# Kernel tuning notes

Measured on AMD Instinct MI355X. Metric: run time of the kernel, lower is better.

The kernel has to match this reference:

```python
import jax, jax.numpy as jnp
import numpy as np

BS = 16384      # batch of tree nodes
N_CH = 8        # children per node (= max_output_degree)
H = 256         # h_size
RANK = 16       # tensor-train rank
N_AGGR = 4      # parallel aggregators
T = 64          # t_size (type embedding dim)
SCALE = 0.05    # param init scale (keeps the length-8 matmul chain stable)


def setup_inputs() -> dict:
    key = jax.random.key(0)
    ks = jax.random.split(key, 8)
    R = (RANK + 1) * RANK
    return {
        "neighbour_h": jax.random.normal(ks[0], (BS, N_CH, H), jnp.float32),
        "type_embs": jax.random.normal(ks[1], (BS, T), jnp.float32),
        "U": jax.random.normal(ks[2], (N_CH, N_AGGR, H, R), jnp.float32) * SCALE,
        "b": jax.random.normal(ks[3], (N_CH, N_AGGR, 1, R), jnp.float32) * SCALE,
        "U_type": jax.random.normal(ks[4], (N_AGGR, T, RANK), jnp.float32) * SCALE,
        "b_type": jax.random.normal(ks[5], (N_AGGR, 1, RANK), jnp.float32) * SCALE,
        "U_output": jax.random.normal(ks[6], (N_AGGR, RANK, H), jnp.float32) * SCALE,
        "b_output": jax.random.normal(ks[7], (N_AGGR, 1, H), jnp.float32) * SCALE,
    }


def reference(neighbour_h, type_embs, U, b, U_type, b_type, U_output, b_output):
    bs, n_ch, h = neighbour_h.shape
    n_aggr, _, rank = U_type.shape

    # per-child projection to TT cores: [bs, n_ch, n_aggr, (rank+1)*rank]
    ris = jnp.einsum('bch,cahr->bcar', neighbour_h, U[:n_ch]) + b[:n_ch, :, 0, :]
    ris = ris.reshape(bs, n_ch, n_aggr, rank + 1, rank)

    # initial rank vector from type embeddings: [bs, n_aggr, rank]
    rank_ris0 = jnp.einsum('bt,atr->bar', type_embs, U_type) + b_type[:, 0, :]

    # sequential TT chain over children (loop-carried dependency) via scan
    xs = jnp.moveaxis(ris, 1, 0)  # [n_ch, bs, n_aggr, rank+1, rank]

    def step(carry, aux):
        U_rank = aux[:, :, :-1, :]   # [bs, n_aggr, rank, rank]
        b_rank = aux[:, :, -2, :]    # row -2 (matches torch's aux[:,:,-2:-1,:])
        return jnp.einsum('bar,barq->baq', carry, U_rank) + b_rank, None

    rank_ris, _ = jax.lax.scan(step, rank_ris0, xs)

    # output projection: [bs, n_aggr, h]
    out = jnp.einsum('bar,arh->bah', rank_ris, U_output) + b_output[:, 0, :]
    return out.reshape(bs, n_aggr * h)
```

## Files before the change

kernel.cpp:

```cpp
#include <hip/hip_runtime.h>


#define N_CH   8
#define H_DIM  256
#define RANK_  16
#define N_AGGR 4
#define T_DIM  64
#define R_FULL 272
#define R_USE  256

typedef __bf16 bf16x8 __attribute__((ext_vector_type(8)));
typedef float  f32x4  __attribute__((ext_vector_type(4)));

union BF8 {
  bf16x8 v;
  unsigned short s[8];
  uint4 q;
};

static __device__ __forceinline__ unsigned short f2bf(float x) {
  union { float f; unsigned int u; } t; t.f = x;
  unsigned int u = t.u;
  return (unsigned short)((u + 0x7FFFu + ((u >> 16) & 1u)) >> 16);
}

__global__ void prep_U_kernel(const float* __restrict__ U, unsigned int* __restrict__ Ubf) {
  unsigned int idx = blockIdx.x * 256u + threadIdx.x;
  unsigned int r  = idx & 255u;
  unsigned int hp = (idx >> 8) & 127u;
  unsigned int ca = idx >> 15;
  const float* src = U + (size_t)(ca * 256u + 2u * hp) * 272u + r;
  unsigned int lo = f2bf(src[0]);
  unsigned int hi = f2bf(src[272]);
  Ubf[(ca * 256u + r) * 128u + hp] = lo | (hi << 16);
}

__global__ __launch_bounds__(256, 1)
void tt_main(const float* __restrict__ nh,
             const float* __restrict__ ty,
             const unsigned short* __restrict__ Ubf,
             const float* __restrict__ bB,
             const float* __restrict__ Ut,
             const float* __restrict__ bt,
             const float* __restrict__ Uo,
             const float* __restrict__ bo,
             float* __restrict__ out)
{
  const int lane = threadIdx.x & 63;
  const int a    = threadIdx.x >> 6;
  const int b0   = blockIdx.x * 64;
  const int lr   = lane & 15;
  const int lg   = lane >> 4;

  f32x4 carry[4];
  {
    float btv = bt[a * 16 + lr];
    BF8 utf[2];
#pragma unroll
    for (int ks = 0; ks < 2; ++ks)
#pragma unroll
      for (int j = 0; j < 8; ++j)
        utf[ks].s[j] = f2bf(Ut[a * 1024 + (ks * 32 + lg * 8 + j) * 16 + lr]);
#pragma unroll
    for (int mt = 0; mt < 4; ++mt) {
      f32x4 acc = { btv, btv, btv, btv };
#pragma unroll
      for (int ks = 0; ks < 2; ++ks) {
        BF8 af;
        const float* src = ty + (size_t)(b0 + mt * 16 + lr) * 64 + ks * 32 + lg * 8;
#pragma unroll
        for (int j = 0; j < 8; ++j) af.s[j] = f2bf(src[j]);
        acc = __builtin_amdgcn_mfma_f32_16x16x32_bf16(af.v, utf[ks].v, acc, 0, 0, 0);
      }
      carry[mt] = acc;
    }
  }

#pragma unroll 1
  for (int c = 0; c < N_CH; ++c) {
    BF8 Af[4][8];
#pragma unroll
    for (int mt = 0; mt < 4; ++mt)
#pragma unroll
      for (int ks = 0; ks < 8; ++ks) {
        const float* src = nh + (size_t)(b0 + mt * 16 + lr) * (N_CH * H_DIM)
                              + c * H_DIM + ks * 32 + lg * 8;
        float4 x0 = *(const float4*)(src);
        float4 x1 = *(const float4*)(src + 4);
        BF8 f;
        f.s[0] = f2bf(x0.x); f.s[1] = f2bf(x0.y); f.s[2] = f2bf(x0.z); f.s[3] = f2bf(x0.w);
        f.s[4] = f2bf(x1.x); f.s[5] = f2bf(x1.y); f.s[6] = f2bf(x1.z); f.s[7] = f2bf(x1.w);
        Af[mt][ks] = f;
      }

    const float* bBc = bB + (c * 4 + a) * R_FULL;
    const unsigned short* Ub = Ubf + (size_t)(c * 4 + a) * 65536;

    f32x4 partial[4];
#pragma unroll
    for (int mt = 0; mt < 4; ++mt) partial[mt] = { 0.f, 0.f, 0.f, 0.f };

    BF8 Bf0[8], Bf1[8];
#pragma unroll
    for (int ks = 0; ks < 8; ++ks)
      Bf0[ks].q = *(const uint4*)(Ub + (size_t)lr * 256 + ks * 32 + lg * 8);

#pragma unroll 1
    for (int tp = 0; tp < 8; ++tp) {
      const int t0 = 2 * tp, t1 = 2 * tp + 1;
#pragma unroll
      for (int ks = 0; ks < 8; ++ks)
        Bf1[ks].q = *(const uint4*)(Ub + (size_t)(t1 * 16 + lr) * 256 + ks * 32 + lg * 8);
      {
        float bias = bBc[t0 * 16 + lr];
        f32x4 acc[4];
#pragma unroll
        for (int mt = 0; mt < 4; ++mt) acc[mt] = { bias, bias, bias, bias };
#pragma unroll
        for (int ks = 0; ks < 8; ++ks)
#pragma unroll
          for (int mt = 0; mt < 4; ++mt)
            acc[mt] = __builtin_amdgcn_mfma_f32_16x16x32_bf16(Af[mt][ks].v, Bf0[ks].v, acc[mt], 0, 0, 0);
        const int srcl = (lane & 48) | t0;
#pragma unroll
        for (int mt = 0; mt < 4; ++mt)
#pragma unroll
          for (int i = 0; i < 4; ++i) {
            float cv = __shfl(carry[mt][i], srcl, 64);
            partial[mt][i] += cv * acc[mt][i];
          }
      }
      if (tp < 7) {
#pragma unroll
        for (int ks = 0; ks < 8; ++ks)
          Bf0[ks].q = *(const uint4*)(Ub + (size_t)((t0 + 2) * 16 + lr) * 256 + ks * 32 + lg * 8);
      }
      {
        float bias = bBc[t1 * 16 + lr];
        float extra = (tp == 7) ? 1.0f : 0.0f;
        f32x4 acc[4];
#pragma unroll
        for (int mt = 0; mt < 4; ++mt) acc[mt] = { bias, bias, bias, bias };
#pragma unroll
        for (int ks = 0; ks < 8; ++ks)
#pragma unroll
          for (int mt = 0; mt < 4; ++mt)
            acc[mt] = __builtin_amdgcn_mfma_f32_16x16x32_bf16(Af[mt][ks].v, Bf1[ks].v, acc[mt], 0, 0, 0);
        const int srcl = (lane & 48) | t1;
#pragma unroll
        for (int mt = 0; mt < 4; ++mt)
#pragma unroll
          for (int i = 0; i < 4; ++i) {
            float cv = __shfl(carry[mt][i], srcl, 64) + extra;
            partial[mt][i] += cv * acc[mt][i];
          }
      }
    }
#pragma unroll
    for (int mt = 0; mt < 4; ++mt) carry[mt] = partial[mt];
  }

  float uo[4][16], bov[4];
#pragma unroll
  for (int chk = 0; chk < 4; ++chk) {
    bov[chk] = bo[a * 256 + chk * 64 + lane];
#pragma unroll
    for (int r = 0; r < 16; ++r)
      uo[chk][r] = Uo[(size_t)a * 4096 + r * 256 + chk * 64 + lane];
  }
#pragma unroll
  for (int mt = 0; mt < 4; ++mt)
#pragma unroll
    for (int g = 0; g < 4; ++g)
#pragma unroll
      for (int i = 0; i < 4; ++i) {
        const int m = mt * 16 + g * 4 + i;
        float cv[16];
#pragma unroll
        for (int r = 0; r < 16; ++r) cv[r] = __shfl(carry[mt][i], (g << 4) | r, 64);
#pragma unroll
        for (int chk = 0; chk < 4; ++chk) {
          float v = bov[chk];
#pragma unroll
          for (int r = 0; r < 16; ++r) v += cv[r] * uo[chk][r];
          out[(size_t)(b0 + m) * 1024 + a * 256 + chk * 64 + lane] = v;
        }
      }
}

extern "C" void kernel_launch(void* const* d_in, const int* in_sizes, int n_in,
                              void* d_out, int out_size, void* d_ws, size_t ws_size,
                              hipStream_t stream) {
  const float* nh = (const float*)d_in[0];
  const float* ty = (const float*)d_in[1];
  const float* U  = (const float*)d_in[2];
  const float* bB = (const float*)d_in[3];
  const float* Ut = (const float*)d_in[4];
  const float* bt = (const float*)d_in[5];
  const float* Uo = (const float*)d_in[6];
  const float* bo = (const float*)d_in[7];
  float* out = (float*)d_out;

  unsigned int* Ubf32 = (unsigned int*)d_ws;

  prep_U_kernel<<<4096, 256, 0, stream>>>(U, Ubf32);
  tt_main<<<256, 256, 0, stream>>>(nh, ty, (const unsigned short*)d_ws,
                                   bB, Ut, bt, Uo, bo, out);
}
```

Measured before the change: 430.2 us.

## Stage bf16 U tiles in LDS via async global_load_lds, 16 waves per block

Blocks now run 1024 threads (16 waves). Each wave owns one aggregator and a 16-row slice, where before each wave covered 64 rows. The neighbour activations are converted to bf16 once per child into LDS. U tiles are staged through double-buffered LDS using global_load_lds, so all waves of a block share one copy instead of each wave fetching its own from global/L2. prep_U is relaid to match the fragment-ordered LDS layout. In exchange the kernel adds a __syncthreads per rank tile, uses 96KB of dynamic LDS, and does fewer MFMAs per B fetch per wave.

```diff
diff --git a/kernel.cpp b/kernel.cpp
--- a/kernel.cpp
+++ b/kernel.cpp
@@ -3,11 +3,7 @@
 
 #define N_CH   8
 #define H_DIM  256
-#define RANK_  16
-#define N_AGGR 4
-#define T_DIM  64
 #define R_FULL 272
-#define R_USE  256
 
 typedef __bf16 bf16x8 __attribute__((ext_vector_type(8)));
 typedef float  f32x4  __attribute__((ext_vector_type(4)));
@@ -18,27 +14,42 @@
   uint4 q;
 };
 
+typedef __attribute__((address_space(3))) unsigned int       lds_u32;
+typedef __attribute__((address_space(1))) const unsigned int glb_u32;
+
 static __device__ __forceinline__ unsigned short f2bf(float x) {
   union { float f; unsigned int u; } t; t.f = x;
   unsigned int u = t.u;
   return (unsigned short)((u + 0x7FFFu + ((u >> 16) & 1u)) >> 16);
 }
+static __device__ __forceinline__ unsigned int pk2(float a, float b) {
+  return (unsigned int)f2bf(a) | ((unsigned int)f2bf(b) << 16);
+}
+static __device__ __forceinline__ void ll16(const void* g, void* l) {
+  __builtin_amdgcn_global_load_lds((glb_u32*)g, (lds_u32*)l, 16, 0, 0);
+}
 
 __global__ void prep_U_kernel(const float* __restrict__ U, unsigned int* __restrict__ Ubf) {
-  unsigned int idx = blockIdx.x * 256u + threadIdx.x;
-  unsigned int r  = idx & 255u;
-  unsigned int hp = (idx >> 8) & 127u;
-  unsigned int ca = idx >> 15;
-  const float* src = U + (size_t)(ca * 256u + 2u * hp) * 272u + r;
-  unsigned int lo = f2bf(src[0]);
-  unsigned int hi = f2bf(src[272]);
-  Ubf[(ca * 256u + r) * 128u + hp] = lo | (hi << 16);
-}
-
-__global__ __launch_bounds__(256, 1)
+  unsigned int idx  = blockIdx.x * 256u + threadIdx.x;
+  unsigned int jp   = idx & 3u;
+  unsigned int lane = (idx >> 2) & 63u;
+  unsigned int ks   = (idx >> 8) & 7u;
+  unsigned int t    = (idx >> 11) & 15u;
+  unsigned int ca   = idx >> 15;
+  unsigned int h = ks * 32u + (lane >> 4) * 8u + jp * 2u;
+  unsigned int r = t * 16u + (lane & 15u);
+  const float* src = U + ((size_t)ca * 256u + h) * R_FULL + r;
+  Ubf[idx] = pk2(src[0], src[R_FULL]);
+}
+
+#define SM_A  0
+#define SM_B0 32768
+#define SM_B1 65536
+
+__global__ __launch_bounds__(1024)
 void tt_main(const float* __restrict__ nh,
              const float* __restrict__ ty,
-             const unsigned short* __restrict__ Ubf,
+             const char*  __restrict__ Ubf,
              const float* __restrict__ bB,
              const float* __restrict__ Ut,
              const float* __restrict__ bt,
@@ -46,118 +57,104 @@
              const float* __restrict__ bo,
              float* __restrict__ out)
 {
-  const int lane = threadIdx.x & 63;
-  const int a    = threadIdx.x >> 6;
+  extern __shared__ char smem[];
+  const int tid  = threadIdx.x;
+  const int lane = tid & 63;
+  const int w    = tid >> 6;
+  const int a    = w & 3;
+  const int sg   = w >> 2;
   const int b0   = blockIdx.x * 64;
+  const int row0 = b0 + sg * 16;
   const int lr   = lane & 15;
   const int lg   = lane >> 4;
 
-  f32x4 carry[4];
+  f32x4 carry;
   {
     float btv = bt[a * 16 + lr];
-    BF8 utf[2];
-#pragma unroll
-    for (int ks = 0; ks < 2; ++ks)
-#pragma unroll
-      for (int j = 0; j < 8; ++j)
-        utf[ks].s[j] = f2bf(Ut[a * 1024 + (ks * 32 + lg * 8 + j) * 16 + lr]);
-#pragma unroll
-    for (int mt = 0; mt < 4; ++mt) {
-      f32x4 acc = { btv, btv, btv, btv };
-#pragma unroll
-      for (int ks = 0; ks < 2; ++ks) {
-        BF8 af;
-        const float* src = ty + (size_t)(b0 + mt * 16 + lr) * 64 + ks * 32 + lg * 8;
-#pragma unroll
-        for (int j = 0; j < 8; ++j) af.s[j] = f2bf(src[j]);
-        acc = __builtin_amdgcn_mfma_f32_16x16x32_bf16(af.v, utf[ks].v, acc, 0, 0, 0);
-      }
-      carry[mt] = acc;
-    }
+    f32x4 acc = { btv, btv, btv, btv };
+#pragma unroll
+    for (int ks = 0; ks < 2; ++ks) {
+      BF8 utf, af;
+#pragma unroll
+      for (int j = 0; j < 8; ++j) {
+        utf.s[j] = f2bf(Ut[a * 1024 + (ks * 32 + lg * 8 + j) * 16 + lr]);
+        af.s[j]  = f2bf(ty[(size_t)(row0 + lr) * 64 + ks * 32 + lg * 8 + j]);
+      }
+      acc = __builtin_amdgcn_mfma_f32_16x16x32_bf16(af.v, utf.v, acc, 0, 0, 0);
+    }
+    carry = acc;
   }
+
+  auto issueB = [&](int c, int t, int bufoff) {
+#pragma unroll
+    for (int q = 0; q < 2; ++q) {
+      const int ch = w * 2 + q;
+      const char* g = Ubf + (((((size_t)c * 4 + (ch >> 3)) * 16 + t) * 8 + (ch & 7)) << 10)
+                          + lane * 16;
+      ll16(g, smem + bufoff + ch * 1024);
+    }
+  };
 
 #pragma unroll 1
   for (int c = 0; c < N_CH; ++c) {
-    BF8 Af[4][8];
-#pragma unroll
-    for (int mt = 0; mt < 4; ++mt)
+    {
+      const int sg_s = tid >> 8;
+      const int ksh  = (tid >> 6) & 3;
+      const int ln   = tid & 63;
+      const int row  = sg_s * 16 + (ln & 15);
+#pragma unroll
+      for (int p = 0; p < 2; ++p) {
+        const int ks = ksh * 2 + p;
+        const int k0 = ks * 32 + (ln >> 4) * 8;
+        const float* s = nh + ((size_t)(b0 + row) * N_CH + c) * H_DIM + k0;
+        float4 x0 = *(const float4*)s;
+        float4 x1 = *(const float4*)(s + 4);
+        uint4 qv;
+        qv.x = pk2(x0.x, x0.y); qv.y = pk2(x0.z, x0.w);
+        qv.z = pk2(x1.x, x1.y); qv.w = pk2(x1.z, x1.w);
+        *(uint4*)(smem + SM_A + ((sg_s * 8 + ks) * 64 + ln) * 16) = qv;
+      }
+    }
+    issueB(c, 0, SM_B0);
+    __syncthreads();
+
+    BF8 Af[8];
+#pragma unroll
+    for (int ks = 0; ks < 8; ++ks)
+      Af[ks].q = *(const uint4*)(smem + SM_A + ((sg * 8 + ks) * 64 + lane) * 16);
+
+    const float* bBp = bB + (c * 4 + a) * R_FULL;
+    float bb[16];
+#pragma unroll
+    for (int t = 0; t < 16; ++t) bb[t] = bBp[t * 16 + lr];
+
+    f32x4 partial = { 0.f, 0.f, 0.f, 0.f };
+
+#pragma unroll 1
+    for (int t = 0; t < 16; ++t) {
+      if (t < 15) issueB(c, t + 1, (t & 1) ? SM_B0 : SM_B1);
+      const int bufoff = (t & 1) ? SM_B1 : SM_B0;
+      float bias = bb[t];
+      f32x4 acc = { bias, bias, bias, bias };
+      uint4 Bq[8];
+#pragma unroll
+      for (int ks = 0; ks < 8; ++ks)
+        Bq[ks] = *(const uint4*)(smem + bufoff + (a * 8 + ks) * 1024 + lane * 16);
 #pragma unroll
       for (int ks = 0; ks < 8; ++ks) {
-        const float* src = nh + (size_t)(b0 + mt * 16 + lr) * (N_CH * H_DIM)
-                              + c * H_DIM + ks * 32 + lg * 8;
-        float4 x0 = *(const float4*)(src);
-        float4 x1 = *(const float4*)(src + 4);
-        BF8 f;
-        f.s[0] = f2bf(x0.x); f.s[1] = f2bf(x0.y); f.s[2] = f2bf(x0.z); f.s[3] = f2bf(x0.w);
-        f.s[4] = f2bf(x1.x); f.s[5] = f2bf(x1.y); f.s[6] = f2bf(x1.z); f.s[7] = f2bf(x1.w);
-        Af[mt][ks] = f;
-      }
-
-    const float* bBc = bB + (c * 4 + a) * R_FULL;
-    const unsigned short* Ub = Ubf + (size_t)(c * 4 + a) * 65536;
-
-    f32x4 partial[4];
-#pragma unroll
-    for (int mt = 0; mt < 4; ++mt) partial[mt] = { 0.f, 0.f, 0.f, 0.f };
-
-    BF8 Bf0[8], Bf1[8];
-#pragma unroll
-    for (int ks = 0; ks < 8; ++ks)
-      Bf0[ks].q = *(const uint4*)(Ub + (size_t)lr * 256 + ks * 32 + lg * 8);
-
-#pragma unroll 1
-    for (int tp = 0; tp < 8; ++tp) {
-      const int t0 = 2 * tp, t1 = 2 * tp + 1;
-#pragma unroll
-      for (int ks = 0; ks < 8; ++ks)
-        Bf1[ks].q = *(const uint4*)(Ub + (size_t)(t1 * 16 + lr) * 256 + ks * 32 + lg * 8);
-      {
-        float bias = bBc[t0 * 16 + lr];
-        f32x4 acc[4];
-#pragma unroll
-        for (int mt = 0; mt < 4; ++mt) acc[mt] = { bias, bias, bias, bias };
-#pragma unroll
-        for (int ks = 0; ks < 8; ++ks)
-#pragma unroll
-          for (int mt = 0; mt < 4; ++mt)
-            acc[mt] = __builtin_amdgcn_mfma_f32_16x16x32_bf16(Af[mt][ks].v, Bf0[ks].v, acc[mt], 0, 0, 0);
-        const int srcl = (lane & 48) | t0;
-#pragma unroll
-        for (int mt = 0; mt < 4; ++mt)
-#pragma unroll
-          for (int i = 0; i < 4; ++i) {
-            float cv = __shfl(carry[mt][i], srcl, 64);
-            partial[mt][i] += cv * acc[mt][i];
-          }
-      }
-      if (tp < 7) {
-#pragma unroll
-        for (int ks = 0; ks < 8; ++ks)
-          Bf0[ks].q = *(const uint4*)(Ub + (size_t)((t0 + 2) * 16 + lr) * 256 + ks * 32 + lg * 8);
-      }
-      {
-        float bias = bBc[t1 * 16 + lr];
-        float extra = (tp == 7) ? 1.0f : 0.0f;
-        f32x4 acc[4];
-#pragma unroll
-        for (int mt = 0; mt < 4; ++mt) acc[mt] = { bias, bias, bias, bias };
-#pragma unroll
-        for (int ks = 0; ks < 8; ++ks)
-#pragma unroll
-          for (int mt = 0; mt < 4; ++mt)
-            acc[mt] = __builtin_amdgcn_mfma_f32_16x16x32_bf16(Af[mt][ks].v, Bf1[ks].v, acc[mt], 0, 0, 0);
-        const int srcl = (lane & 48) | t1;
-#pragma unroll
-        for (int mt = 0; mt < 4; ++mt)
-#pragma unroll
-          for (int i = 0; i < 4; ++i) {
-            float cv = __shfl(carry[mt][i], srcl, 64) + extra;
-            partial[mt][i] += cv * acc[mt][i];
-          }
-      }
-    }
-#pragma unroll
-    for (int mt = 0; mt < 4; ++mt) carry[mt] = partial[mt];
+        BF8 bf; bf.q = Bq[ks];
+        acc = __builtin_amdgcn_mfma_f32_16x16x32_bf16(Af[ks].v, bf.v, acc, 0, 0, 0);
+      }
+      const float extra = (t == 15) ? 1.0f : 0.0f;
+      const int   srcl  = (lane & 48) | t;
+#pragma unroll
+      for (int i = 0; i < 4; ++i) {
+        float cv = __shfl(carry[i], srcl, 64) + extra;
+        partial[i] += cv * acc[i];
+      }
+      __syncthreads();
+    }
+    carry = partial;
   }
 
   float uo[4][16], bov[4];
@@ -169,23 +166,21 @@
       uo[chk][r] = Uo[(size_t)a * 4096 + r * 256 + chk * 64 + lane];
   }
 #pragma unroll
-  for (int mt = 0; mt < 4; ++mt)
-#pragma unroll
-    for (int g = 0; g < 4; ++g)
-#pragma unroll
-      for (int i = 0; i < 4; ++i) {
-        const int m = mt * 16 + g * 4 + i;
-        float cv[16];
-#pragma unroll
-        for (int r = 0; r < 16; ++r) cv[r] = __shfl(carry[mt][i], (g << 4) | r, 64);
-#pragma unroll
-        for (int chk = 0; chk < 4; ++chk) {
-          float v = bov[chk];
-#pragma unroll
-          for (int r = 0; r < 16; ++r) v += cv[r] * uo[chk][r];
-          out[(size_t)(b0 + m) * 1024 + a * 256 + chk * 64 + lane] = v;
-        }
-      }
+  for (int g = 0; g < 4; ++g)
+#pragma unroll
+    for (int i = 0; i < 4; ++i) {
+      const int m = g * 4 + i;
+      float cv[16];
+#pragma unroll
+      for (int r = 0; r < 16; ++r) cv[r] = __shfl(carry[i], (g << 4) | r, 64);
+#pragma unroll
+      for (int chk = 0; chk < 4; ++chk) {
+        float v = bov[chk];
+#pragma unroll
+        for (int r = 0; r < 16; ++r) v += cv[r] * uo[chk][r];
+        out[(size_t)(row0 + m) * 1024 + a * 256 + chk * 64 + lane] = v;
+      }
+    }
 }
 
 extern "C" void kernel_launch(void* const* d_in, const int* in_sizes, int n_in,
@@ -204,6 +199,11 @@
   unsigned int* Ubf32 = (unsigned int*)d_ws;
 
   prep_U_kernel<<<4096, 256, 0, stream>>>(U, Ubf32);
-  tt_main<<<256, 256, 0, stream>>>(nh, ty, (const unsigned short*)d_ws,
-                                   bB, Ut, bt, Uo, bo, out);
-}
+
+  static int smem_set = 0;
+  (void)hipFuncSetAttribute((const void*)tt_main,
+                            hipFuncAttributeMaxDynamicSharedMemorySize, 98304);
+  (void)smem_set;
+  tt_main<<<256, 1024, 98304, stream>>>(nh, ty, (const char*)d_ws,
+                                        bB, Ut, bt, Uo, bo, out);
+}
```

Measured after the change: 372.3 us. 1.16x faster.
